# Kernel tuning notes

Hardware: AMD Instinct MI355X
Metric: run time of the kernel (lower is better)

Reference implementation:

```python
import jax, jax.numpy as jnp
import numpy as np

IN_FEATURES = 1024
OUT_FEATURES = 1280
K = 16  # intermediate_features
B_EXTRA = OUT_FEATURES - IN_FEATURES  # 256
N = 256


def setup_inputs() -> dict:
    key = jax.random.key(0)
    k1, k2 = jax.random.split(key)
    x = jax.random.normal(k1, (N, IN_FEATURES), dtype=jnp.float32)
    T = jax.random.normal(k2, (IN_FEATURES, B_EXTRA, K), dtype=jnp.float32) * 0.02
    return {"x": x, "T": T}


def reference(x, T):
    # M: (N, B_extra, K)
    M = jnp.einsum('ni,ibk->nbk', x, T)
    # pairwise L1 over K: (N, N, B_extra)
    l1 = jnp.abs(M[:, None, :, :] - M[None, :, :, :]).sum(axis=3)
    # sum over the other-sample axis, subtract self term exp(0)=1
    out = jnp.exp(-l1).sum(axis=0) - 1.0  # (N, B_extra)
    return jnp.concatenate([x, out], axis=1)  # (N, OUT_FEATURES)
```

## Files before the change

### kernel.cpp

```cpp
#include <hip/hip_runtime.h>
#include <hip/hip_fp16.h>
#include <hip/hip_bf16.h>

#define NB 256
#define IN_F 1024
#define BEX 256
#define KD 16
#define NJ 4096
#define OUT_F 1280

typedef short bf16x8 __attribute__((ext_vector_type(8)));
typedef float f32x4 __attribute__((ext_vector_type(4)));
typedef _Float16 h2 __attribute__((ext_vector_type(2)));

__device__ inline unsigned short f2bf(float f) {
    __hip_bfloat16 h = __float2bfloat16(f);
    return *reinterpret_cast<unsigned short*>(&h);
}

__device__ inline void cp16(const void* g, void* l) {
    __builtin_amdgcn_global_load_lds((const __attribute__((address_space(1))) void*)g,
                                     (__attribute__((address_space(3))) void*)l, 16, 0, 0);
}

__global__ __launch_bounds__(256) void k_prep(const float* __restrict__ x,
                                              const float* __restrict__ T,
                                              float* __restrict__ out,
                                              unsigned short* __restrict__ x_bf,
                                              unsigned short* __restrict__ Tt) {
    const int bid = blockIdx.x;
    const int t = threadIdx.x;
    if (bid < 4096) {
        __shared__ float tile[32][33];
        const int j0 = (bid & 127) * 32;
        const int i0 = (bid >> 7) * 32;
        {
            const int r = t >> 3, cg = (t & 7) << 2;
            float4 v = *(const float4*)(T + (size_t)(i0 + r) * NJ + j0 + cg);
            tile[r][cg + 0] = v.x; tile[r][cg + 1] = v.y;
            tile[r][cg + 2] = v.z; tile[r][cg + 3] = v.w;
        }
        __syncthreads();
        const int jr = t >> 3, ig = (t & 7) << 2;
        ushort4 o;
        o.x = f2bf(tile[ig + 0][jr]);
        o.y = f2bf(tile[ig + 1][jr]);
        o.z = f2bf(tile[ig + 2][jr]);
        o.w = f2bf(tile[ig + 3][jr]);
        *(ushort4*)(Tt + (size_t)(j0 + jr) * IN_F + i0 + ig) = o;
    } else {
        const int r = bid - 4096;
        float4 v = *(const float4*)(x + (size_t)r * IN_F + t * 4);
        *(float4*)(out + (size_t)r * OUT_F + t * 4) = v;
        ushort4 o;
        o.x = f2bf(v.x); o.y = f2bf(v.y); o.z = f2bf(v.z); o.w = f2bf(v.w);
        *(ushort4*)(x_bf + (size_t)r * IN_F + t * 4) = o;
        if (t < 64)
            *(float4*)(out + (size_t)r * OUT_F + IN_F + t * 4) =
                make_float4(-1.f, -1.f, -1.f, -1.f);
    }
}

__global__ __launch_bounds__(256) void k_gemm(const unsigned short* __restrict__ A,
                                              const unsigned short* __restrict__ B,
                                              __half* __restrict__ M2h) {
    __shared__ unsigned short lds[4][64 * 128];
    const int t = threadIdx.x;
    const int w = t >> 6, l = t & 63;
    const int n0 = blockIdx.y * 64;
    const int j0 = blockIdx.x * 64;

    const unsigned short* aA[4];
    const unsigned short* aB[4];
    int lofs[4];
    #pragma unroll
    for (int p = 0; p < 4; ++p) {
        int s = t + p * 256;
        int r = s >> 4;
        int kg = (s & 15) ^ (r & 15);
        aA[p] = A + (size_t)(n0 + r) * IN_F + kg * 8;
        aB[p] = B + (size_t)(j0 + r) * IN_F + kg * 8;
        lofs[p] = s * 8;
    }

    f32x4 acc[2][2];
    #pragma unroll
    for (int i = 0; i < 2; ++i)
        #pragma unroll
        for (int j = 0; j < 2; ++j)
            acc[i][j] = (f32x4){0.f, 0.f, 0.f, 0.f};

    #pragma unroll
    for (int p = 0; p < 4; ++p) cp16(aA[p], &lds[0][lofs[p]]);
    #pragma unroll
    for (int p = 0; p < 4; ++p) cp16(aB[p], &lds[1][lofs[p]]);

    const int rowA0 = ((w & 1) * 32 + (l & 15)) * 128;
    const int rowA1 = rowA0 + 16 * 128;
    const int rowB0 = (((w >> 1) & 1) * 32 + (l & 15)) * 128;
    const int rowB1 = rowB0 + 16 * 128;

    for (int s = 0; s < 8; ++s) {
        __syncthreads();
        if (s < 7) {
            const int k0 = (s + 1) * 128;
            const int bsel = ((s + 1) & 1) * 2;
            #pragma unroll
            for (int p = 0; p < 4; ++p) cp16(aA[p] + k0, &lds[bsel + 0][lofs[p]]);
            #pragma unroll
            for (int p = 0; p < 4; ++p) cp16(aB[p] + k0, &lds[bsel + 1][lofs[p]]);
        }
        const unsigned short* La = lds[(s & 1) * 2 + 0];
        const unsigned short* Lb = lds[(s & 1) * 2 + 1];
        #pragma unroll
        for (int kk = 0; kk < 4; ++kk) {
            const int kg = kk * 4 + (l >> 4);
            const int ks = (kg ^ (l & 15)) * 8;
            bf16x8 a0 = *(const bf16x8*)&La[rowA0 + ks];
            bf16x8 a1 = *(const bf16x8*)&La[rowA1 + ks];
            bf16x8 b0 = *(const bf16x8*)&Lb[rowB0 + ks];
            bf16x8 b1 = *(const bf16x8*)&Lb[rowB1 + ks];
            acc[0][0] = __builtin_amdgcn_mfma_f32_16x16x32_bf16(a0, b0, acc[0][0], 0, 0, 0);
            acc[0][1] = __builtin_amdgcn_mfma_f32_16x16x32_bf16(a0, b1, acc[0][1], 0, 0, 0);
            acc[1][0] = __builtin_amdgcn_mfma_f32_16x16x32_bf16(a1, b0, acc[1][0], 0, 0, 0);
            acc[1][1] = __builtin_amdgcn_mfma_f32_16x16x32_bf16(a1, b1, acc[1][1], 0, 0, 0);
        }
    }

    const int col = l & 15;
    #pragma unroll
    for (int nt = 0; nt < 2; ++nt) {
        #pragma unroll
        for (int jt = 0; jt < 2; ++jt) {
            const int jc = j0 + ((w >> 1) & 1) * 32 + jt * 16 + col;
            const int b = jc >> 4;
            const int k = jc & 15;
            __half* base = M2h + (size_t)b * (NB * KD) + k;
            #pragma unroll
            for (int r = 0; r < 4; ++r) {
                const int n = n0 + (w & 1) * 32 + nt * 16 + (l >> 4) * 4 + r;
                base[n * KD] = __float2half(acc[nt][jt][r]);
            }
        }
    }
}

union U8 { float4 f4[2]; h2 h[8]; };

__global__ __launch_bounds__(256) void k_pairwise(const __half* __restrict__ M2h,
                                                  float* __restrict__ out) {
    __shared__ __half rows[128 * KD];
    __shared__ float part[256 * 4];
    const int b = blockIdx.x;
    const int mh = blockIdx.y;
    const int t = threadIdx.x;
    const int qg = t & 63, ms = t >> 6;
    const __half* Mb = M2h + (size_t)b * (NB * KD);

    ((float4*)rows)[t] = ((const float4*)(Mb + mh * 128 * KD))[t];

    U8 q[4];
    #pragma unroll
    for (int r = 0; r < 4; ++r) {
        const __half* qp = Mb + (qg * 4 + r) * KD;
        q[r].f4[0] = *(const float4*)(qp);
        q[r].f4[1] = *(const float4*)(qp + 8);
    }
    __syncthreads();

    const h2 one = {(_Float16)1.0f, (_Float16)1.0f};
    float e[4] = {0.f, 0.f, 0.f, 0.f};

    #pragma unroll 2
    for (int m = 0; m < 32; ++m) {
        U8 p;
        const __half* rp = rows + (ms * 32 + m) * KD;
        p.f4[0] = *(const float4*)(rp);
        p.f4[1] = *(const float4*)(rp + 8);
        #pragma unroll
        for (int r = 0; r < 4; ++r) {
            float l0 = 0.f, l1 = 0.f;
            #pragma unroll
            for (int i = 0; i < 8; i += 2) {
                h2 d0 = q[r].h[i] - p.h[i];
                h2 d1 = q[r].h[i + 1] - p.h[i + 1];
                unsigned u0 = (*(unsigned*)&d0) & 0x7FFF7FFFu;
                unsigned u1 = (*(unsigned*)&d1) & 0x7FFF7FFFu;
                l0 = __builtin_amdgcn_fdot2(*(h2*)&u0, one, l0, false);
                l1 = __builtin_amdgcn_fdot2(*(h2*)&u1, one, l1, false);
            }
            e[r] += __expf(-(l0 + l1));
        }
    }

    #pragma unroll
    for (int r = 0; r < 4; ++r)
        part[(qg * 4 + r) * 4 + ms] = e[r];
    __syncthreads();

    float4 p4 = ((const float4*)part)[t];
    atomicAdd(&out[(size_t)t * OUT_F + IN_F + b], p4.x + p4.y + p4.z + p4.w);
}

extern "C" void kernel_launch(void* const* d_in, const int* in_sizes, int n_in,
                              void* d_out, int out_size, void* d_ws, size_t ws_size,
                              hipStream_t stream) {
    const float* x = (const float*)d_in[0];
    const float* T = (const float*)d_in[1];
    float* out = (float*)d_out;

    char* ws = (char*)d_ws;
    unsigned short* x_bf = (unsigned short*)ws;
    unsigned short* Tt   = (unsigned short*)(ws + (1u << 19));
    __half* M2h          = (__half*)(ws + (1u << 19) + (1u << 23));

    k_prep<<<dim3(4352), dim3(256), 0, stream>>>(x, T, out, x_bf, Tt);
    k_gemm<<<dim3(64, 4), dim3(256), 0, stream>>>(x_bf, Tt, M2h);
    k_pairwise<<<dim3(256, 2), dim3(256), 0, stream>>>(M2h, out);
}
```

Measured before the change: 95.74 us.

## Fuse projection GEMM and pairwise kernel per feature block, drop T transpose pass

Removes the separate T transpose/convert pass and the global GEMM kernel. Each of 256 blocks (one per extra feature b) now loads its 1024x16 slice of T straight into swizzled LDS as bf16, computes M for all 256 samples with MFMA, keeps M in LDS, and runs the pairwise exp-L1 sum there. Results are written directly with the self-term subtracted, so the -1 init and the atomics are gone. The cost is that every block re-reads all of x_bf from global/L2, each block's T loads are strided, and there are only 256 blocks of 512 threads.

```diff
diff --git a/kernel.cpp b/kernel.cpp
--- a/kernel.cpp
+++ b/kernel.cpp
@@ -18,156 +18,75 @@
     return *reinterpret_cast<unsigned short*>(&h);
 }
 
-__device__ inline void cp16(const void* g, void* l) {
-    __builtin_amdgcn_global_load_lds((const __attribute__((address_space(1))) void*)g,
-                                     (__attribute__((address_space(3))) void*)l, 16, 0, 0);
+union U8 { float4 f4[2]; h2 h[8]; };
+
+__global__ __launch_bounds__(256) void k_prep(const float* __restrict__ x,
+                                              float* __restrict__ out,
+                                              unsigned short* __restrict__ x_bf) {
+    const int r = blockIdx.x, t = threadIdx.x;
+    float4 v = *(const float4*)(x + (size_t)r * IN_F + t * 4);
+    *(float4*)(out + (size_t)r * OUT_F + t * 4) = v;
+    ushort4 o;
+    o.x = f2bf(v.x); o.y = f2bf(v.y); o.z = f2bf(v.z); o.w = f2bf(v.w);
+    *(ushort4*)(x_bf + (size_t)r * IN_F + t * 4) = o;
 }
 
-__global__ __launch_bounds__(256) void k_prep(const float* __restrict__ x,
-                                              const float* __restrict__ T,
-                                              float* __restrict__ out,
-                                              unsigned short* __restrict__ x_bf,
-                                              unsigned short* __restrict__ Tt) {
-    const int bid = blockIdx.x;
-    const int t = threadIdx.x;
-    if (bid < 4096) {
-        __shared__ float tile[32][33];
-        const int j0 = (bid & 127) * 32;
-        const int i0 = (bid >> 7) * 32;
-        {
-            const int r = t >> 3, cg = (t & 7) << 2;
-            float4 v = *(const float4*)(T + (size_t)(i0 + r) * NJ + j0 + cg);
-            tile[r][cg + 0] = v.x; tile[r][cg + 1] = v.y;
-            tile[r][cg + 2] = v.z; tile[r][cg + 3] = v.w;
-        }
-        __syncthreads();
-        const int jr = t >> 3, ig = (t & 7) << 2;
-        ushort4 o;
-        o.x = f2bf(tile[ig + 0][jr]);
-        o.y = f2bf(tile[ig + 1][jr]);
-        o.z = f2bf(tile[ig + 2][jr]);
-        o.w = f2bf(tile[ig + 3][jr]);
-        *(ushort4*)(Tt + (size_t)(j0 + jr) * IN_F + i0 + ig) = o;
-    } else {
-        const int r = bid - 4096;
-        float4 v = *(const float4*)(x + (size_t)r * IN_F + t * 4);
-        *(float4*)(out + (size_t)r * OUT_F + t * 4) = v;
-        ushort4 o;
-        o.x = f2bf(v.x); o.y = f2bf(v.y); o.z = f2bf(v.z); o.w = f2bf(v.w);
-        *(ushort4*)(x_bf + (size_t)r * IN_F + t * 4) = o;
-        if (t < 64)
-            *(float4*)(out + (size_t)r * OUT_F + IN_F + t * 4) =
-                make_float4(-1.f, -1.f, -1.f, -1.f);
-    }
-}
+__global__ __launch_bounds__(512) void k_fused(const float* __restrict__ T,
+                                               const unsigned short* __restrict__ x_bf,
+                                               float* __restrict__ out) {
+    __shared__ unsigned short TsT[16 * 1024];
+    __shared__ __half rows[NB * KD];
+    __shared__ float part[NB * 8];
 
-__global__ __launch_bounds__(256) void k_gemm(const unsigned short* __restrict__ A,
-                                              const unsigned short* __restrict__ B,
-                                              __half* __restrict__ M2h) {
-    __shared__ unsigned short lds[4][64 * 128];
+    const int b = blockIdx.x;
     const int t = threadIdx.x;
     const int w = t >> 6, l = t & 63;
-    const int n0 = blockIdx.y * 64;
-    const int j0 = blockIdx.x * 64;
 
-    const unsigned short* aA[4];
-    const unsigned short* aB[4];
-    int lofs[4];
     #pragma unroll
-    for (int p = 0; p < 4; ++p) {
-        int s = t + p * 256;
-        int r = s >> 4;
-        int kg = (s & 15) ^ (r & 15);
-        aA[p] = A + (size_t)(n0 + r) * IN_F + kg * 8;
-        aB[p] = B + (size_t)(j0 + r) * IN_F + kg * 8;
-        lofs[p] = s * 8;
+    for (int p = 0; p < 8; ++p) {
+        const int g = p * 512 + t;
+        const int i = g >> 2, c4 = g & 3;
+        float4 v = *(const float4*)(T + (size_t)i * NJ + b * KD + c4 * 4);
+        const float f[4] = {v.x, v.y, v.z, v.w};
+        #pragma unroll
+        for (int jj = 0; jj < 4; ++jj) {
+            const int kp = c4 * 4 + jj;
+            TsT[kp * 1024 + (((i >> 3) ^ (kp & 7)) << 3) + (i & 7)] = f2bf(f[jj]);
+        }
+    }
+    __syncthreads();
+
+    f32x4 acc0 = {0.f, 0.f, 0.f, 0.f}, acc1 = {0.f, 0.f, 0.f, 0.f};
+    const int kp = l & 15;
+    const int lr = l >> 4;
+    const unsigned short* ap = x_bf + (size_t)(w * 32 + kp) * IN_F + lr * 8;
+    const unsigned short* Tb = &TsT[kp * 1024];
+    #pragma unroll 8
+    for (int s = 0; s < 32; ++s) {
+        const int ch = s * 4 + lr;
+        bf16x8 bf = *(const bf16x8*)&Tb[(ch ^ (kp & 7)) << 3];
+        bf16x8 a0 = *(const bf16x8*)(ap + s * 32);
+        bf16x8 a1 = *(const bf16x8*)(ap + 16 * IN_F + s * 32);
+        acc0 = __builtin_amdgcn_mfma_f32_16x16x32_bf16(a0, bf, acc0, 0, 0, 0);
+        acc1 = __builtin_amdgcn_mfma_f32_16x16x32_bf16(a1, bf, acc1, 0, 0, 0);
     }
 
-    f32x4 acc[2][2];
     #pragma unroll
-    for (int i = 0; i < 2; ++i)
-        #pragma unroll
-        for (int j = 0; j < 2; ++j)
-            acc[i][j] = (f32x4){0.f, 0.f, 0.f, 0.f};
+    for (int r = 0; r < 4; ++r) {
+        const int n0 = w * 32 + lr * 4 + r;
+        rows[n0 * KD + kp] = __float2half(acc0[r]);
+        rows[(n0 + 16) * KD + kp] = __float2half(acc1[r]);
+    }
+    __syncthreads();
 
-    #pragma unroll
-    for (int p = 0; p < 4; ++p) cp16(aA[p], &lds[0][lofs[p]]);
-    #pragma unroll
-    for (int p = 0; p < 4; ++p) cp16(aB[p], &lds[1][lofs[p]]);
-
-    const int rowA0 = ((w & 1) * 32 + (l & 15)) * 128;
-    const int rowA1 = rowA0 + 16 * 128;
-    const int rowB0 = (((w >> 1) & 1) * 32 + (l & 15)) * 128;
-    const int rowB1 = rowB0 + 16 * 128;
-
-    for (int s = 0; s < 8; ++s) {
-        __syncthreads();
-        if (s < 7) {
-            const int k0 = (s + 1) * 128;
-            const int bsel = ((s + 1) & 1) * 2;
-            #pragma unroll
-            for (int p = 0; p < 4; ++p) cp16(aA[p] + k0, &lds[bsel + 0][lofs[p]]);
-            #pragma unroll
-            for (int p = 0; p < 4; ++p) cp16(aB[p] + k0, &lds[bsel + 1][lofs[p]]);
-        }
-        const unsigned short* La = lds[(s & 1) * 2 + 0];
-        const unsigned short* Lb = lds[(s & 1) * 2 + 1];
-        #pragma unroll
-        for (int kk = 0; kk < 4; ++kk) {
-            const int kg = kk * 4 + (l >> 4);
-            const int ks = (kg ^ (l & 15)) * 8;
-            bf16x8 a0 = *(const bf16x8*)&La[rowA0 + ks];
-            bf16x8 a1 = *(const bf16x8*)&La[rowA1 + ks];
-            bf16x8 b0 = *(const bf16x8*)&Lb[rowB0 + ks];
-            bf16x8 b1 = *(const bf16x8*)&Lb[rowB1 + ks];
-            acc[0][0] = __builtin_amdgcn_mfma_f32_16x16x32_bf16(a0, b0, acc[0][0], 0, 0, 0);
-            acc[0][1] = __builtin_amdgcn_mfma_f32_16x16x32_bf16(a0, b1, acc[0][1], 0, 0, 0);
-            acc[1][0] = __builtin_amdgcn_mfma_f32_16x16x32_bf16(a1, b0, acc[1][0], 0, 0, 0);
-            acc[1][1] = __builtin_amdgcn_mfma_f32_16x16x32_bf16(a1, b1, acc[1][1], 0, 0, 0);
-        }
-    }
-
-    const int col = l & 15;
-    #pragma unroll
-    for (int nt = 0; nt < 2; ++nt) {
-        #pragma unroll
-        for (int jt = 0; jt < 2; ++jt) {
-            const int jc = j0 + ((w >> 1) & 1) * 32 + jt * 16 + col;
-            const int b = jc >> 4;
-            const int k = jc & 15;
-            __half* base = M2h + (size_t)b * (NB * KD) + k;
-            #pragma unroll
-            for (int r = 0; r < 4; ++r) {
-                const int n = n0 + (w & 1) * 32 + nt * 16 + (l >> 4) * 4 + r;
-                base[n * KD] = __float2half(acc[nt][jt][r]);
-            }
-        }
-    }
-}
-
-union U8 { float4 f4[2]; h2 h[8]; };
-
-__global__ __launch_bounds__(256) void k_pairwise(const __half* __restrict__ M2h,
-                                                  float* __restrict__ out) {
-    __shared__ __half rows[128 * KD];
-    __shared__ float part[256 * 4];
-    const int b = blockIdx.x;
-    const int mh = blockIdx.y;
-    const int t = threadIdx.x;
-    const int qg = t & 63, ms = t >> 6;
-    const __half* Mb = M2h + (size_t)b * (NB * KD);
-
-    ((float4*)rows)[t] = ((const float4*)(Mb + mh * 128 * KD))[t];
-
+    const int qg = l, ms = w;
     U8 q[4];
     #pragma unroll
     for (int r = 0; r < 4; ++r) {
-        const __half* qp = Mb + (qg * 4 + r) * KD;
+        const __half* qp = rows + (qg * 4 + r) * KD;
         q[r].f4[0] = *(const float4*)(qp);
         q[r].f4[1] = *(const float4*)(qp + 8);
     }
-    __syncthreads();
-
     const h2 one = {(_Float16)1.0f, (_Float16)1.0f};
     float e[4] = {0.f, 0.f, 0.f, 0.f};
 
@@ -195,11 +114,15 @@
 
     #pragma unroll
     for (int r = 0; r < 4; ++r)
-        part[(qg * 4 + r) * 4 + ms] = e[r];
+        part[(qg * 4 + r) * 8 + ms] = e[r];
     __syncthreads();
 
-    float4 p4 = ((const float4*)part)[t];
-    atomicAdd(&out[(size_t)t * OUT_F + IN_F + b], p4.x + p4.y + p4.z + p4.w);
+    if (t < NB) {
+        float4 pa = ((const float4*)part)[t * 2];
+        float4 pb = ((const float4*)part)[t * 2 + 1];
+        out[(size_t)t * OUT_F + IN_F + b] =
+            (pa.x + pa.y + pa.z + pa.w + pb.x + pb.y + pb.z + pb.w) - 1.0f;
+    }
 }
 
 extern "C" void kernel_launch(void* const* d_in, const int* in_sizes, int n_in,
@@ -209,12 +132,8 @@
     const float* T = (const float*)d_in[1];
     float* out = (float*)d_out;
 
-    char* ws = (char*)d_ws;
-    unsigned short* x_bf = (unsigned short*)ws;
-    unsigned short* Tt   = (unsigned short*)(ws + (1u << 19));
-    __half* M2h          = (__half*)(ws + (1u << 19) + (1u << 23));
+    unsigned short* x_bf = (unsigned short*)d_ws;
 
-    k_prep<<<dim3(4352), dim3(256), 0, stream>>>(x, T, out, x_bf, Tt);
-    k_gemm<<<dim3(64, 4), dim3(256), 0, stream>>>(x_bf, Tt, M2h);
-    k_pairwise<<<dim3(256, 2), dim3(256), 0, stream>>>(M2h, out);
+    k_prep<<<dim3(256), dim3(256), 0, stream>>>(x, out, x_bf);
+    k_fused<<<dim3(256), dim3(512), 0, stream>>>(T, x_bf, out);
 }
```

Result: slower. 102.3 us (+6.8%).

## Exploit L1 symmetry in pairwise kernel with upper-triangular tiling

Applied to the files above, without the earlier changes.

Restructures the pairwise kernel into one 512-thread block per feature column. The block loads all 256 rows into swizzled LDS and computes only the upper-triangular 64x64 tiles. Each exp(-L1) value is added to both the row sum and, through shuffle reductions into a shared column-sum array, the column sum. This roughly halves the fp16 diff/dot and exp work. It also drops the cross-block atomicAdd and the -1 initialisation in the prep kernel, since the final value is written directly. The trade-off is fewer, larger blocks and extra shuffle/LDS reduction traffic.

```diff
diff --git a/kernel.cpp b/kernel.cpp
--- a/kernel.cpp
+++ b/kernel.cpp
@@ -22,6 +22,8 @@
     __builtin_amdgcn_global_load_lds((const __attribute__((address_space(1))) void*)g,
                                      (__attribute__((address_space(3))) void*)l, 16, 0, 0);
 }
+
+union U8 { float4 f4[2]; h2 h[8]; };
 
 __global__ __launch_bounds__(256) void k_prep(const float* __restrict__ x,
                                               const float* __restrict__ T,
@@ -55,9 +57,6 @@
         ushort4 o;
         o.x = f2bf(v.x); o.y = f2bf(v.y); o.z = f2bf(v.z); o.w = f2bf(v.w);
         *(ushort4*)(x_bf + (size_t)r * IN_F + t * 4) = o;
-        if (t < 64)
-            *(float4*)(out + (size_t)r * OUT_F + IN_F + t * 4) =
-                make_float4(-1.f, -1.f, -1.f, -1.f);
     }
 }
 
@@ -133,9 +132,9 @@
         #pragma unroll
         for (int jt = 0; jt < 2; ++jt) {
             const int jc = j0 + ((w >> 1) & 1) * 32 + jt * 16 + col;
-            const int b = jc >> 4;
+            const int bb = jc >> 4;
             const int k = jc & 15;
-            __half* base = M2h + (size_t)b * (NB * KD) + k;
+            __half* base = M2h + (size_t)bb * (NB * KD) + k;
             #pragma unroll
             for (int r = 0; r < 4; ++r) {
                 const int n = n0 + (w & 1) * 32 + nt * 16 + (l >> 4) * 4 + r;
@@ -145,61 +144,105 @@
     }
 }
 
-union U8 { float4 f4[2]; h2 h[8]; };
-
-__global__ __launch_bounds__(256) void k_pairwise(const __half* __restrict__ M2h,
+__global__ __launch_bounds__(512) void k_pairwise(const __half* __restrict__ M2h,
                                                   float* __restrict__ out) {
-    __shared__ __half rows[128 * KD];
-    __shared__ float part[256 * 4];
+    __shared__ __half rows[NB * KD];
+    __shared__ float Sm[NB];
+    __shared__ float part[NB * 8];
     const int b = blockIdx.x;
-    const int mh = blockIdx.y;
     const int t = threadIdx.x;
-    const int qg = t & 63, ms = t >> 6;
+    const int lane = t & 63, w = t >> 6;
+    const int qq = t & 15;
+    const int mm = t >> 4;
     const __half* Mb = M2h + (size_t)b * (NB * KD);
 
-    ((float4*)rows)[t] = ((const float4*)(Mb + mh * 128 * KD))[t];
-
-    U8 q[4];
-    #pragma unroll
-    for (int r = 0; r < 4; ++r) {
-        const __half* qp = Mb + (qg * 4 + r) * KD;
-        q[r].f4[0] = *(const float4*)(qp);
-        q[r].f4[1] = *(const float4*)(qp + 8);
-    }
+    {
+        float4 v = ((const float4*)Mb)[t];
+        ((float4*)rows)[t ^ ((t >> 3) & 7)] = v;
+    }
+    if (t < NB) Sm[t] = 0.f;
     __syncthreads();
 
     const h2 one = {(_Float16)1.0f, (_Float16)1.0f};
-    float e[4] = {0.f, 0.f, 0.f, 0.f};
-
-    #pragma unroll 2
-    for (int m = 0; m < 32; ++m) {
-        U8 p;
-        const __half* rp = rows + (ms * 32 + m) * KD;
-        p.f4[0] = *(const float4*)(rp);
-        p.f4[1] = *(const float4*)(rp + 8);
+
+    #pragma unroll
+    for (int ti = 0; ti < 4; ++ti) {
+        U8 q[4];
         #pragma unroll
         for (int r = 0; r < 4; ++r) {
-            float l0 = 0.f, l1 = 0.f;
-            #pragma unroll
-            for (int i = 0; i < 8; i += 2) {
-                h2 d0 = q[r].h[i] - p.h[i];
-                h2 d1 = q[r].h[i + 1] - p.h[i + 1];
-                unsigned u0 = (*(unsigned*)&d0) & 0x7FFF7FFFu;
-                unsigned u1 = (*(unsigned*)&d1) & 0x7FFF7FFFu;
-                l0 = __builtin_amdgcn_fdot2(*(h2*)&u0, one, l0, false);
-                l1 = __builtin_amdgcn_fdot2(*(h2*)&u1, one, l1, false);
+            const int n = ti * 64 + qq * 4 + r;
+            const int sw = (n >> 2) & 7;
+            q[r].f4[0] = ((const float4*)rows)[(n * 2) ^ sw];
+            q[r].f4[1] = ((const float4*)rows)[(n * 2 + 1) ^ sw];
+        }
+        float eq[4] = {0.f, 0.f, 0.f, 0.f};
+
+        for (int tj = ti; tj < 4; ++tj) {
+            const int m0 = tj * 64 + mm * 2;
+            const int sw = (m0 >> 2) & 7;
+            U8 p0, p1;
+            p0.f4[0] = ((const float4*)rows)[(m0 * 2) ^ sw];
+            p0.f4[1] = ((const float4*)rows)[(m0 * 2 + 1) ^ sw];
+            p1.f4[0] = ((const float4*)rows)[(m0 * 2 + 2) ^ sw];
+            p1.f4[1] = ((const float4*)rows)[(m0 * 2 + 3) ^ sw];
+
+            float pm0 = 0.f, pm1 = 0.f;
+            #pragma unroll
+            for (int r = 0; r < 4; ++r) {
+                float a0 = 0.f, a1 = 0.f, b0 = 0.f, b1 = 0.f;
+                #pragma unroll
+                for (int i = 0; i < 8; i += 2) {
+                    h2 d0 = q[r].h[i] - p0.h[i];
+                    h2 d1 = q[r].h[i + 1] - p0.h[i + 1];
+                    h2 d2 = q[r].h[i] - p1.h[i];
+                    h2 d3 = q[r].h[i + 1] - p1.h[i + 1];
+                    unsigned u0 = (*(unsigned*)&d0) & 0x7FFF7FFFu;
+                    unsigned u1 = (*(unsigned*)&d1) & 0x7FFF7FFFu;
+                    unsigned u2 = (*(unsigned*)&d2) & 0x7FFF7FFFu;
+                    unsigned u3 = (*(unsigned*)&d3) & 0x7FFF7FFFu;
+                    a0 = __builtin_amdgcn_fdot2(*(h2*)&u0, one, a0, false);
+                    a1 = __builtin_amdgcn_fdot2(*(h2*)&u1, one, a1, false);
+                    b0 = __builtin_amdgcn_fdot2(*(h2*)&u2, one, b0, false);
+                    b1 = __builtin_amdgcn_fdot2(*(h2*)&u3, one, b1, false);
+                }
+                const float e0 = __expf(-(a0 + a1));
+                const float e1 = __expf(-(b0 + b1));
+                eq[r] += e0 + e1;
+                pm0 += e0;
+                pm1 += e1;
             }
-            e[r] += __expf(-(l0 + l1));
-        }
-    }
-
-    #pragma unroll
-    for (int r = 0; r < 4; ++r)
-        part[(qg * 4 + r) * 4 + ms] = e[r];
+            if (tj > ti) {
+                #pragma unroll
+                for (int s = 1; s < 16; s <<= 1) {
+                    pm0 += __shfl_xor(pm0, s);
+                    pm1 += __shfl_xor(pm1, s);
+                }
+                if (qq == 0) {
+                    Sm[m0] += pm0;
+                    Sm[m0 + 1] += pm1;
+                }
+            }
+        }
+        #pragma unroll
+        for (int r = 0; r < 4; ++r) {
+            eq[r] += __shfl_xor(eq[r], 16);
+            eq[r] += __shfl_xor(eq[r], 32);
+        }
+        if (lane < 16) {
+            #pragma unroll
+            for (int r = 0; r < 4; ++r)
+                part[(ti * 64 + lane * 4 + r) * 8 + w] = eq[r];
+        }
+    }
     __syncthreads();
 
-    float4 p4 = ((const float4*)part)[t];
-    atomicAdd(&out[(size_t)t * OUT_F + IN_F + b], p4.x + p4.y + p4.z + p4.w);
+    if (t < NB) {
+        const float* pp = &part[t * 8];
+        float s = Sm[t] - 1.f;
+        #pragma unroll
+        for (int i = 0; i < 8; ++i) s += pp[i];
+        out[(size_t)t * OUT_F + IN_F + b] = s;
+    }
 }
 
 extern "C" void kernel_launch(void* const* d_in, const int* in_sizes, int n_in,
@@ -216,5 +259,5 @@
 
     k_prep<<<dim3(4352), dim3(256), 0, stream>>>(x, T, out, x_bf, Tt);
     k_gemm<<<dim3(64, 4), dim3(256), 0, stream>>>(x_bf, Tt, M2h);
-    k_pairwise<<<dim3(256, 2), dim3(256), 0, stream>>>(M2h, out);
-}
+    k_pairwise<<<dim3(256), dim3(512), 0, stream>>>(M2h, out);
+}
```

Result: faster. 91.49 us, median of 3 (-4.4%).

## Restructure pairwise kernel: full-row LDS tile, 8-lane split, shuffle reduce, no atomics

Applied to the files above, without the earlier changes.

The pairwise kernel now loads all 256 rows for a feature into XOR-swizzled LDS and launches 8 query slices per feature. Each query row is handled by 8 lanes that each cover 32 partner rows, and the lanes combine their sums with xor shuffles. The result is written directly with the -1 applied, so the -1 initialisation in prep and the global atomics are no longer needed. This gives more blocks and less register state per thread. The cost is more redundant LDS fills across blocks, since each block loads the whole 256-row tile for its feature.

```diff
diff --git a/kernel.cpp b/kernel.cpp
--- a/kernel.cpp
+++ b/kernel.cpp
@@ -22,6 +22,8 @@
     __builtin_amdgcn_global_load_lds((const __attribute__((address_space(1))) void*)g,
                                      (__attribute__((address_space(3))) void*)l, 16, 0, 0);
 }
+
+union U8 { float4 f4[2]; h2 h[8]; };
 
 __global__ __launch_bounds__(256) void k_prep(const float* __restrict__ x,
                                               const float* __restrict__ T,
@@ -55,9 +57,6 @@
         ushort4 o;
         o.x = f2bf(v.x); o.y = f2bf(v.y); o.z = f2bf(v.z); o.w = f2bf(v.w);
         *(ushort4*)(x_bf + (size_t)r * IN_F + t * 4) = o;
-        if (t < 64)
-            *(float4*)(out + (size_t)r * OUT_F + IN_F + t * 4) =
-                make_float4(-1.f, -1.f, -1.f, -1.f);
     }
 }
 
@@ -133,9 +132,9 @@
         #pragma unroll
         for (int jt = 0; jt < 2; ++jt) {
             const int jc = j0 + ((w >> 1) & 1) * 32 + jt * 16 + col;
-            const int b = jc >> 4;
+            const int bb = jc >> 4;
             const int k = jc & 15;
-            __half* base = M2h + (size_t)b * (NB * KD) + k;
+            __half* base = M2h + (size_t)bb * (NB * KD) + k;
             #pragma unroll
             for (int r = 0; r < 4; ++r) {
                 const int n = n0 + (w & 1) * 32 + nt * 16 + (l >> 4) * 4 + r;
@@ -145,61 +144,58 @@
     }
 }
 
-union U8 { float4 f4[2]; h2 h[8]; };
-
-__global__ __launch_bounds__(256) void k_pairwise(const __half* __restrict__ M2h,
-                                                  float* __restrict__ out) {
-    __shared__ __half rows[128 * KD];
-    __shared__ float part[256 * 4];
+__global__ __launch_bounds__(256, 8) void k_pairwise(const __half* __restrict__ M2h,
+                                                     float* __restrict__ out) {
+    __shared__ __half rows[NB * KD];
     const int b = blockIdx.x;
-    const int mh = blockIdx.y;
+    const int slice = blockIdx.y;
     const int t = threadIdx.x;
-    const int qg = t & 63, ms = t >> 6;
+    const int s = t & 7;
+    const int qr = t >> 3;
     const __half* Mb = M2h + (size_t)b * (NB * KD);
 
-    ((float4*)rows)[t] = ((const float4*)(Mb + mh * 128 * KD))[t];
-
-    U8 q[4];
-    #pragma unroll
-    for (int r = 0; r < 4; ++r) {
-        const __half* qp = Mb + (qg * 4 + r) * KD;
-        q[r].f4[0] = *(const float4*)(qp);
-        q[r].f4[1] = *(const float4*)(qp + 8);
+    {
+        const int u0 = 2 * t, u1 = 2 * t + 1;
+        ((float4*)rows)[u0 ^ ((u0 >> 6) & 7)] = ((const float4*)Mb)[u0];
+        ((float4*)rows)[u1 ^ ((u1 >> 6) & 7)] = ((const float4*)Mb)[u1];
     }
     __syncthreads();
 
+    U8 q;
+    {
+        const int u = (slice * 32 + qr) * 2;
+        const int g = (u >> 6) & 7;
+        q.f4[0] = ((const float4*)rows)[u ^ g];
+        q.f4[1] = ((const float4*)rows)[(u + 1) ^ g];
+    }
+
     const h2 one = {(_Float16)1.0f, (_Float16)1.0f};
-    float e[4] = {0.f, 0.f, 0.f, 0.f};
-
-    #pragma unroll 2
-    for (int m = 0; m < 32; ++m) {
+    const float4* R = (const float4*)rows + s * 64;
+    float e = 0.f;
+
+    #pragma unroll 4
+    for (int j = 0; j < 32; ++j) {
         U8 p;
-        const __half* rp = rows + (ms * 32 + m) * KD;
-        p.f4[0] = *(const float4*)(rp);
-        p.f4[1] = *(const float4*)(rp + 8);
-        #pragma unroll
-        for (int r = 0; r < 4; ++r) {
-            float l0 = 0.f, l1 = 0.f;
-            #pragma unroll
-            for (int i = 0; i < 8; i += 2) {
-                h2 d0 = q[r].h[i] - p.h[i];
-                h2 d1 = q[r].h[i + 1] - p.h[i + 1];
-                unsigned u0 = (*(unsigned*)&d0) & 0x7FFF7FFFu;
-                unsigned u1 = (*(unsigned*)&d1) & 0x7FFF7FFFu;
-                l0 = __builtin_amdgcn_fdot2(*(h2*)&u0, one, l0, false);
-                l1 = __builtin_amdgcn_fdot2(*(h2*)&u1, one, l1, false);
-            }
-            e[r] += __expf(-(l0 + l1));
-        }
-    }
-
-    #pragma unroll
-    for (int r = 0; r < 4; ++r)
-        part[(qg * 4 + r) * 4 + ms] = e[r];
-    __syncthreads();
-
-    float4 p4 = ((const float4*)part)[t];
-    atomicAdd(&out[(size_t)t * OUT_F + IN_F + b], p4.x + p4.y + p4.z + p4.w);
+        p.f4[0] = R[(2 * j) ^ s];
+        p.f4[1] = R[(2 * j + 1) ^ s];
+        float l0 = 0.f, l1 = 0.f;
+        #pragma unroll
+        for (int i = 0; i < 8; i += 2) {
+            h2 d0 = q.h[i] - p.h[i];
+            h2 d1 = q.h[i + 1] - p.h[i + 1];
+            unsigned w0 = (*(unsigned*)&d0) & 0x7FFF7FFFu;
+            unsigned w1 = (*(unsigned*)&d1) & 0x7FFF7FFFu;
+            l0 = __builtin_amdgcn_fdot2(*(h2*)&w0, one, l0, false);
+            l1 = __builtin_amdgcn_fdot2(*(h2*)&w1, one, l1, false);
+        }
+        e += __expf(-(l0 + l1));
+    }
+
+    e += __shfl_xor(e, 1);
+    e += __shfl_xor(e, 2);
+    e += __shfl_xor(e, 4);
+    if (s == 0)
+        out[(size_t)(slice * 32 + qr) * OUT_F + IN_F + b] = e - 1.f;
 }
 
 extern "C" void kernel_launch(void* const* d_in, const int* in_sizes, int n_in,
@@ -216,5 +212,5 @@
 
     k_prep<<<dim3(4352), dim3(256), 0, stream>>>(x, T, out, x_bf, Tt);
     k_gemm<<<dim3(64, 4), dim3(256), 0, stream>>>(x_bf, Tt, M2h);
-    k_pairwise<<<dim3(256, 2), dim3(256), 0, stream>>>(M2h, out);
-}
+    k_pairwise<<<dim3(256, 8), dim3(256), 0, stream>>>(M2h, out);
+}
```

Measured after the change: 95.12 us. No clear change (-0.6%).
